# Performance work log

Measured on AMD Instinct MI355X. Metric: run time of the kernel, lower is better.

## Reference

```python
import jax, jax.numpy as jnp
import numpy as np

N, IN, H, C, E = 20000, 256, 256, 16, 640000

def sage_conv(x, edge_index, W_l, b_l, W_r):
    # PyG SAGEConv (aggr='mean', root_weight=True):
    # out = lin_l(mean_{j in N(i)} x_j) + lin_r(x_i)
    src, dst = edge_index[0], edge_index[1]
    n = x.shape[0]
    msgs = x[src]                                            # [E, d] irregular gather
    agg = jax.ops.segment_sum(msgs, dst, num_segments=n)     # [N, d]
    deg = jax.ops.segment_sum(jnp.ones((msgs.shape[0],), x.dtype), dst, num_segments=n)
    agg = agg / jnp.maximum(deg, 1.0)[:, None]               # mean aggregation
    return agg @ W_l + b_l + x @ W_r


def setup_inputs() -> dict:
    key = jax.random.key(0)
    ks = jax.random.split(key, 10)
    s = lambda k, fi, fo: jax.random.normal(k, (fi, fo), jnp.float32) / np.sqrt(fi)
    return {
        "x": jax.random.normal(ks[0], (N, IN), jnp.float32),
        "edge_index": jax.random.randint(ks[1], (2, E), 0, N, jnp.int64),
        "W1l": s(ks[2], IN, H), "b1": jnp.zeros((H,), jnp.float32), "W1r": s(ks[3], IN, H),
        "W2l": s(ks[4], H, H),  "b2": jnp.zeros((H,), jnp.float32), "W2r": s(ks[5], H, H),
        "Wc": s(ks[6], H, C),   "bc": jnp.zeros((C,), jnp.float32),
    }


def reference(x, edge_index, W1l, b1, W1r, W2l, b2, W2r, Wc, bc):
    h = sage_conv(x, edge_index, W1l, b1, W1r)
    h = jax.nn.relu(h)                    # dropout is identity in eval mode
    z = sage_conv(h, edge_index, W2l, b2, W2r)
    return z @ Wc + bc                    # classifier logits [N, C]
```

## Files before the change

### kernel.cpp

```cpp
#include <hip/hip_runtime.h>
#include <hip/hip_bf16.h>


#define FEAT 256
#define NCLS 16
#define ZPAD 264
#define NSH  8
#define SCAP 64
#define SLOTS (NSH * SCAP)
#define CAPTOT 128

typedef __bf16 bf16x8 __attribute__((ext_vector_type(8)));
typedef __bf16 bf16x4 __attribute__((ext_vector_type(4)));
typedef float  f32x4  __attribute__((ext_vector_type(4)));
typedef float  f32x2  __attribute__((ext_vector_type(2)));
typedef unsigned int uint4v __attribute__((ext_vector_type(4)));

#define ACC8(S, U) do {                                                   \
    _Pragma("unroll")                                                     \
    for (int w_ = 0; w_ < 4; ++w_) {                                      \
        f32x2 lo_ = __builtin_amdgcn_cvt_pk_f32_fp8(U[w_], false);        \
        f32x2 hi_ = __builtin_amdgcn_cvt_pk_f32_fp8(U[w_], true);         \
        S[w_][0] += lo_[0]; S[w_][1] += lo_[1];                           \
        S[w_][2] += hi_[0]; S[w_][3] += hi_[1];                           \
    } } while (0)

__device__ __forceinline__ void load_entries(
    const int* __restrict__ cnt, const unsigned short* __restrict__ bucket,
    int node, int lane, int& e0, int& e1, int& deg, float& inv)
{
    int4 ca = *(const int4*)(cnt + node * NSH);
    int4 cb = *(const int4*)(cnt + node * NSH + 4);
    int cs[NSH] = {ca.x, ca.y, ca.z, ca.w, cb.x, cb.y, cb.z, cb.w};
    int ctrue = 0, d = 0;
    #pragma unroll
    for (int s = 0; s < NSH; ++s) {
        ctrue += cs[s];
        cs[s] = cs[s] < SCAP ? cs[s] : SCAP;
        d += cs[s];
    }
    deg = d < CAPTOT ? d : CAPTOT;
    inv = ctrue > 0 ? 1.0f / (float)ctrue : 0.0f;
    const unsigned short* lst = bucket + (size_t)node * SLOTS;

    auto get = [&](int i) -> int {
        int s = 0, loc = i;
        #pragma unroll
        for (int t = 0; t < NSH - 1; ++t) {
            if (s == t && loc >= cs[t]) { loc -= cs[t]; s = t + 1; }
        }
        return lst[s * SCAP + loc];
    };
    e0 = (lane < deg)      ? get(lane)      : 0;
    e1 = (lane + 64 < deg) ? get(lane + 64) : 0;
}


__global__ void combo_kernel(const float* __restrict__ x,
                             const float* __restrict__ W1l, const float* __restrict__ W1r,
                             const float* __restrict__ W2l, const float* __restrict__ W2r,
                             const float* __restrict__ Wc, const float* __restrict__ b2,
                             const float* __restrict__ bc,
                             const int* __restrict__ src, const int* __restrict__ dst,
                             __bf16* __restrict__ xb, unsigned char* __restrict__ x8,
                             __bf16* __restrict__ W1lT, __bf16* __restrict__ W1rT,
                             __bf16* __restrict__ WaT, __bf16* __restrict__ WbT,
                             float* __restrict__ bc2,
                             int* __restrict__ cnt, unsigned short* __restrict__ bucket,
                             int n4, int E, int nb_cvt) {
    int t = threadIdx.x;
    int bx = blockIdx.x;
    if (bx < nb_cvt) {
        int i = bx * 256 + t;
        if (i < n4) {
            f32x4 v = ((const f32x4*)x)[i];
            bf16x4 o;
            #pragma unroll
            for (int j = 0; j < 4; ++j) o[j] = (__bf16)v[j];
            ((bf16x4*)xb)[i] = o;
            int pk = 0;
            pk = __builtin_amdgcn_cvt_pk_fp8_f32(v[0], v[1], pk, false);
            pk = __builtin_amdgcn_cvt_pk_fp8_f32(v[2], v[3], pk, true);
            ((int*)x8)[i] = pk;
        }
    } else if (bx < nb_cvt + 512) {
        int b = bx - nb_cvt;
        int w = b >> 8, nn = b & 255;
        const float* W = w ? W1r : W1l;
        __bf16* WT = w ? W1rT : W1lT;
        WT[nn * FEAT + t] = (__bf16)W[t * FEAT + nn];
    } else if (bx < nb_cvt + 512 + 32) {
        int b = bx - nb_cvt - 512;
        int c = b & 15;
        const float* W = (b < 16) ? W2l : W2r;
        __bf16* WT = (b < 16) ? WaT : WbT;
        float s = 0.f;
        #pragma unroll 4
        for (int m = 0; m < FEAT; ++m)
            s += W[t * FEAT + m] * Wc[m * NCLS + c];
        WT[c * FEAT + t] = (__bf16)s;
    } else if (bx == nb_cvt + 512 + 32) {
        if (t < NCLS) {
            float s = 0.f;
            for (int k = 0; k < FEAT; ++k) s += b2[k] * Wc[k * NCLS + t];
            bc2[t] = s + bc[t];
        }
    } else {
        int sh = bx & (NSH - 1);
        int idx = (bx - nb_cvt - 512 - 33) * 256 + t;
        int e2 = idx * 2;
        if (e2 < E) {
            int2 sv = *(const int2*)(src + e2);
            int2 dv = *(const int2*)(dst + e2);
            int p0 = atomicAdd(&cnt[dv.x * NSH + sh], 1);
            if (p0 < SCAP) bucket[(size_t)dv.x * SLOTS + sh * SCAP + p0] = (unsigned short)sv.x;
            if (e2 + 1 < E) {
                int p1 = atomicAdd(&cnt[dv.y * NSH + sh], 1);
                if (p1 < SCAP) bucket[(size_t)dv.y * SLOTS + sh * SCAP + p1] = (unsigned short)sv.y;
            }
        }
    }
}


__global__ __launch_bounds__(256) void agg_gemm_kernel(
    const unsigned char* __restrict__ t8, const int* __restrict__ cnt,
    const unsigned short* __restrict__ bucket,
    const __bf16* __restrict__ A2,
    const __bf16* __restrict__ B1T, const __bf16* __restrict__ B2T,
    const float* __restrict__ bias,
    const __bf16* __restrict__ WaT, const __bf16* __restrict__ WbT,
    const float* __restrict__ bc2,
    __bf16* __restrict__ pb, float* __restrict__ q, int M)
{
    __shared__ __align__(16) __bf16 tile[32][ZPAD];

    int m0   = blockIdx.x * 32;
    int lane = threadIdx.x & 63;
    int wave = threadIdx.x >> 6;
    int l16  = lane & 15, quad = lane >> 4;

    #pragma unroll 1
    for (int nd = 0; nd < 8; ++nd) {
        int row  = wave * 8 + nd;
        int node = m0 + row;
        if (node < M) {
            int e0, e1, deg; float inv;
            load_entries(cnt, bucket, node, lane, e0, e1, deg, inv);

            f32x4 s0[4], s1[4];
            #pragma unroll
            for (int w = 0; w < 4; ++w) { s0[w] = (f32x4){0.f,0.f,0.f,0.f}; s1[w] = (f32x4){0.f,0.f,0.f,0.f}; }

            int nfull = deg >> 2;
            int rem   = deg & 3;
            const unsigned char* base = t8 + l16 * 16;

            int tt = 0;
            for (; tt + 3 < nfull; tt += 4) {
                int i0 = (tt + 0) * 4 + quad, i1 = (tt + 1) * 4 + quad;
                int i2 = (tt + 2) * 4 + quad, i3 = (tt + 3) * 4 + quad;
                int j0 = (i0 < 64) ? __shfl(e0, i0) : __shfl(e1, i0 - 64);
                int j1 = (i1 < 64) ? __shfl(e0, i1) : __shfl(e1, i1 - 64);
                int j2 = (i2 < 64) ? __shfl(e0, i2) : __shfl(e1, i2 - 64);
                int j3 = (i3 < 64) ? __shfl(e0, i3) : __shfl(e1, i3 - 64);
                uint4v u0 = *(const uint4v*)(base + (size_t)j0 * FEAT);
                uint4v u1 = *(const uint4v*)(base + (size_t)j1 * FEAT);
                uint4v u2 = *(const uint4v*)(base + (size_t)j2 * FEAT);
                uint4v u3 = *(const uint4v*)(base + (size_t)j3 * FEAT);
                ACC8(s0, u0); ACC8(s1, u1); ACC8(s0, u2); ACC8(s1, u3);
            }
            for (; tt < nfull; ++tt) {
                int i = tt * 4 + quad;
                int j = (i < 64) ? __shfl(e0, i) : __shfl(e1, i - 64);
                uint4v u = *(const uint4v*)(base + (size_t)j * FEAT);
                ACC8(s0, u);
            }
            if (rem) {
                int i = nfull * 4 + quad;
                int j = (i < 64) ? __shfl(e0, i) : __shfl(e1, i - 64);
                if (quad < rem) {
                    uint4v u = *(const uint4v*)(base + (size_t)j * FEAT);
                    ACC8(s1, u);
                }
            }

            #pragma unroll
            for (int w = 0; w < 4; ++w)
                #pragma unroll
                for (int j = 0; j < 4; ++j) {
                    float v = s0[w][j] + s1[w][j];
                    v += __shfl_xor(v, 16, 64);
                    v += __shfl_xor(v, 32, 64);
                    s0[w][j] = v;
                }

            bf16x4 o;
            #pragma unroll
            for (int j = 0; j < 4; ++j) o[j] = (__bf16)(s0[quad][j] * inv);
            *(bf16x4*)(&tile[row][l16 * 16 + quad * 4]) = o;
        } else {
            bf16x4 z = (bf16x4){(__bf16)0.f, (__bf16)0.f, (__bf16)0.f, (__bf16)0.f};
            *(bf16x4*)(&tile[row][l16 * 16 + quad * 4]) = z;
        }
    }
    __syncthreads();

    f32x4 acc[2][4];
    #pragma unroll
    for (int a = 0; a < 2; ++a)
        #pragma unroll
        for (int b = 0; b < 4; ++b) acc[a][b] = (f32x4){0.f, 0.f, 0.f, 0.f};

    int arow[2];
    #pragma unroll
    for (int mt = 0; mt < 2; ++mt) {
        int r = m0 + mt * 16 + l16;
        arow[mt] = (r < M) ? r : (M - 1);
    }
    int nbase = wave * 64;

    #pragma unroll 2
    for (int kk = 0; kk < 8; ++kk) {
        int k0 = kk * 32 + quad * 8;
        bf16x8 af[2], bfm[4];
        #pragma unroll
        for (int mt = 0; mt < 2; ++mt)
            af[mt] = *(const bf16x8*)(&tile[mt * 16 + l16][k0]);
        #pragma unroll
        for (int nt = 0; nt < 4; ++nt)
            bfm[nt] = *(const bf16x8*)(B1T + (size_t)(nbase + nt * 16 + l16) * FEAT + k0);
        #pragma unroll
        for (int mt = 0; mt < 2; ++mt)
            #pragma unroll
            for (int nt = 0; nt < 4; ++nt)
                acc[mt][nt] = __builtin_amdgcn_mfma_f32_16x16x32_bf16(
                    af[mt], bfm[nt], acc[mt][nt], 0, 0, 0);
    }
    __syncthreads();

    #pragma unroll 2
    for (int kk = 0; kk < 8; ++kk) {
        int k0 = kk * 32 + quad * 8;
        bf16x8 af[2], bfm[4];
        #pragma unroll
        for (int mt = 0; mt < 2; ++mt)
            af[mt] = *(const bf16x8*)(A2 + (size_t)arow[mt] * FEAT + k0);
        #pragma unroll
        for (int nt = 0; nt < 4; ++nt)
            bfm[nt] = *(const bf16x8*)(B2T + (size_t)(nbase + nt * 16 + l16) * FEAT + k0);
        #pragma unroll
        for (int mt = 0; mt < 2; ++mt)
            #pragma unroll
            for (int nt = 0; nt < 4; ++nt)
                acc[mt][nt] = __builtin_amdgcn_mfma_f32_16x16x32_bf16(
                    af[mt], bfm[nt], acc[mt][nt], 0, 0, 0);
    }

    #pragma unroll
    for (int nt = 0; nt < 4; ++nt) {
        int col = nbase + nt * 16 + l16;
        float bv = bias[col];
        #pragma unroll
        for (int mt = 0; mt < 2; ++mt) {
            int lr = mt * 16 + quad * 4;
            #pragma unroll
            for (int r = 0; r < 4; ++r) {
                float v = acc[mt][nt][r] + bv;
                tile[lr + r][col] = (__bf16)(v > 0.f ? v : 0.f);
            }
        }
    }
    __syncthreads();

    {
        int half = wave >> 1;
        int lr = half * 16 + l16;
        const __bf16* WT = (wave & 1) ? WbT : WaT;
        f32x4 a = {0.f, 0.f, 0.f, 0.f};
        #pragma unroll
        for (int kk = 0; kk < 8; ++kk) {
            int k0 = kk * 32 + quad * 8;
            bf16x8 av = *(const bf16x8*)(&tile[lr][k0]);
            bf16x8 bv = *(const bf16x8*)(WT + (size_t)l16 * FEAT + k0);
            a = __builtin_amdgcn_mfma_f32_16x16x32_bf16(av, bv, a, 0, 0, 0);
        }
        if (wave & 1) {
            float qv = bc2[l16];
            #pragma unroll
            for (int r = 0; r < 4; ++r) {
                int row = m0 + half * 16 + quad * 4 + r;
                if (row < M) q[(size_t)row * NCLS + l16] = a[r] + qv;
            }
        } else {
            #pragma unroll
            for (int r = 0; r < 4; ++r) {
                int row = m0 + half * 16 + quad * 4 + r;
                if (row < M) pb[(size_t)row * NCLS + l16] = (__bf16)a[r];
            }
        }
    }
}


__global__ __launch_bounds__(256) void agg_out_kernel(
    const __bf16* __restrict__ pb, const float* __restrict__ q,
    const int* __restrict__ cnt, const unsigned short* __restrict__ bucket,
    float* __restrict__ out, int n)
{
    int wave = threadIdx.x >> 6;
    int node = blockIdx.x * 4 + wave;
    if (node >= n) return;
    int lane = threadIdx.x & 63;
    int quad = lane >> 4, l16 = lane & 15;

    int e0, e1, deg; float inv;
    load_entries(cnt, bucket, node, lane, e0, e1, deg, inv);

    float s0 = 0.f, s1 = 0.f;
    int nfull = deg >> 2;
    int rem   = deg & 3;

    int tt = 0;
    for (; tt + 3 < nfull; tt += 4) {
        int i0 = (tt + 0) * 4 + quad, i1 = (tt + 1) * 4 + quad;
        int i2 = (tt + 2) * 4 + quad, i3 = (tt + 3) * 4 + quad;
        int j0 = (i0 < 64) ? __shfl(e0, i0) : __shfl(e1, i0 - 64);
        int j1 = (i1 < 64) ? __shfl(e0, i1) : __shfl(e1, i1 - 64);
        int j2 = (i2 < 64) ? __shfl(e0, i2) : __shfl(e1, i2 - 64);
        int j3 = (i3 < 64) ? __shfl(e0, i3) : __shfl(e1, i3 - 64);
        float v0 = (float)pb[(size_t)j0 * NCLS + l16];
        float v1 = (float)pb[(size_t)j1 * NCLS + l16];
        float v2 = (float)pb[(size_t)j2 * NCLS + l16];
        float v3 = (float)pb[(size_t)j3 * NCLS + l16];
        s0 += v0 + v1;
        s1 += v2 + v3;
    }
    for (; tt < nfull; ++tt) {
        int i = tt * 4 + quad;
        int j = (i < 64) ? __shfl(e0, i) : __shfl(e1, i - 64);
        s0 += (float)pb[(size_t)j * NCLS + l16];
    }
    if (rem) {
        int i = nfull * 4 + quad;
        int j = (i < 64) ? __shfl(e0, i) : __shfl(e1, i - 64);
        if (quad < rem) s1 += (float)pb[(size_t)j * NCLS + l16];
    }

    float v = s0 + s1;
    v += __shfl_xor(v, 16, 64);
    v += __shfl_xor(v, 32, 64);

    if (quad == 0) {
        out[(size_t)node * NCLS + l16] = v * inv + q[(size_t)node * NCLS + l16];
    }
}


extern "C" void kernel_launch(void* const* d_in, const int* in_sizes, int n_in,
                              void* d_out, int out_size, void* d_ws, size_t ws_size,
                              hipStream_t stream) {
    const float* x   = (const float*)d_in[0];
    const int*   ei  = (const int*)d_in[1];
    const float* W1l = (const float*)d_in[2];
    const float* b1  = (const float*)d_in[3];
    const float* W1r = (const float*)d_in[4];
    const float* W2l = (const float*)d_in[5];
    const float* b2  = (const float*)d_in[6];
    const float* W2r = (const float*)d_in[7];
    const float* Wc  = (const float*)d_in[8];
    const float* bc  = (const float*)d_in[9];
    float* out = (float*)d_out;

    const int n = in_sizes[0] / FEAT;
    const int E = in_sizes[1] / 2;
    const int* srcp = ei;
    const int* dstp = ei + E;

    char* p = (char*)d_ws;
    auto alloc = [&](size_t bytes) { char* r = p; p += (bytes + 511) & ~511ull; return r; };
    int* cnt       = (int*)alloc((size_t)n * NSH * 4);
    unsigned short* bucket = (unsigned short*)alloc((size_t)n * SLOTS * 2);
    __bf16* W1lT   = (__bf16*)alloc((size_t)FEAT * FEAT * 2);
    __bf16* W1rT   = (__bf16*)alloc((size_t)FEAT * FEAT * 2);
    __bf16* WaT    = (__bf16*)alloc((size_t)NCLS * FEAT * 2);
    __bf16* WbT    = (__bf16*)alloc((size_t)NCLS * FEAT * 2);
    float*  bc2    = (float*)alloc((size_t)NCLS * 4);
    __bf16* xb     = (__bf16*)alloc((size_t)n * FEAT * 2);
    unsigned char* x8 = (unsigned char*)alloc((size_t)n * FEAT);
    __bf16* pb     = (__bf16*)alloc((size_t)n * NCLS * 2);
    float*  qb     = (float*)alloc((size_t)n * NCLS * 4);

    int n4 = n * FEAT / 4;
    int nb_cvt  = (n4 + 255) / 256;
    int nb_edge = (E + 511) / 512;

    hipMemsetAsync(cnt, 0, (size_t)n * NSH * 4, stream);

    combo_kernel<<<nb_cvt + 512 + 32 + 1 + nb_edge, 256, 0, stream>>>(
        x, W1l, W1r, W2l, W2r, Wc, b2, bc, srcp, dstp,
        xb, x8, W1lT, W1rT, WaT, WbT, bc2, cnt, bucket, n4, E, nb_cvt);

    agg_gemm_kernel<<<(n + 31) / 32, 256, 0, stream>>>(
        x8, cnt, bucket, xb, W1lT, W1rT, b1, WaT, WbT, bc2, pb, qb, n);

    agg_out_kernel<<<(n + 3) / 4, 256, 0, stream>>>(pb, qb, cnt, bucket, out, n);
}
```

Before: 221.2 us.

## Halve agg_gemm row tile and overlap root GEMM with aggregation barrier

Shrinks the per-block row tile of the fused aggregate+GEMM kernel from 32 to 16 nodes, doubling the grid to improve load balance and occupancy across CUs. It also moves the root-weight GEMM (x @ W_r from global memory) ahead of the first barrier so it runs before waiting for the shared-memory aggregation tile. The trade-off is that weight matrices get reloaded by twice as many blocks, and only two of four waves do the final classifier projection.

After: 208.5 us. 1.06x faster.

```diff
diff --git a/kernel.cpp b/kernel.cpp
--- a/kernel.cpp
+++ b/kernel.cpp
@@ -5,6 +5,7 @@
 #define FEAT 256
 #define NCLS 16
 #define ZPAD 264
+#define MT   16
 #define NSH  8
 #define SCAP 64
 #define SLOTS (NSH * SCAP)
@@ -133,16 +134,16 @@
     const float* __restrict__ bc2,
     __bf16* __restrict__ pb, float* __restrict__ q, int M)
 {
-    __shared__ __align__(16) __bf16 tile[32][ZPAD];
-
-    int m0   = blockIdx.x * 32;
+    __shared__ __align__(16) __bf16 tile[MT][ZPAD];
+
+    int m0   = blockIdx.x * MT;
     int lane = threadIdx.x & 63;
     int wave = threadIdx.x >> 6;
     int l16  = lane & 15, quad = lane >> 4;
 
     #pragma unroll 1
-    for (int nd = 0; nd < 8; ++nd) {
-        int row  = wave * 8 + nd;
+    for (int nd = 0; nd < 4; ++nd) {
+        int row  = wave * 4 + nd;
         int node = m0 + row;
         if (node < M) {
             int e0, e1, deg; float inv;
@@ -204,99 +205,79 @@
             *(bf16x4*)(&tile[row][l16 * 16 + quad * 4]) = z;
         }
     }
-    __syncthreads();
-
-    f32x4 acc[2][4];
+
+    f32x4 acc[4];
     #pragma unroll
-    for (int a = 0; a < 2; ++a)
-        #pragma unroll
-        for (int b = 0; b < 4; ++b) acc[a][b] = (f32x4){0.f, 0.f, 0.f, 0.f};
-
-    int arow[2];
-    #pragma unroll
-    for (int mt = 0; mt < 2; ++mt) {
-        int r = m0 + mt * 16 + l16;
-        arow[mt] = (r < M) ? r : (M - 1);
-    }
+    for (int b = 0; b < 4; ++b) acc[b] = (f32x4){0.f, 0.f, 0.f, 0.f};
+
+    int r = m0 + l16;
+    int arow = (r < M) ? r : (M - 1);
     int nbase = wave * 64;
 
     #pragma unroll 2
     for (int kk = 0; kk < 8; ++kk) {
         int k0 = kk * 32 + quad * 8;
-        bf16x8 af[2], bfm[4];
-        #pragma unroll
-        for (int mt = 0; mt < 2; ++mt)
-            af[mt] = *(const bf16x8*)(&tile[mt * 16 + l16][k0]);
+        bf16x8 af = *(const bf16x8*)(A2 + (size_t)arow * FEAT + k0);
+        bf16x8 bfm[4];
         #pragma unroll
         for (int nt = 0; nt < 4; ++nt)
-            bfm[nt] = *(const bf16x8*)(B1T + (size_t)(nbase + nt * 16 + l16) * FEAT + k0);
-        #pragma unroll
-        for (int mt = 0; mt < 2; ++mt)
-            #pragma unroll
-            for (int nt = 0; nt < 4; ++nt)
-                acc[mt][nt] = __builtin_amdgcn_mfma_f32_16x16x32_bf16(
-                    af[mt], bfm[nt], acc[mt][nt], 0, 0, 0);
-    }
+            bfm[nt] = *(const bf16x8*)(B2T + (size_t)(nbase + nt * 16 + l16) * FEAT + k0);
+        #pragma unroll
+        for (int nt = 0; nt < 4; ++nt)
+            acc[nt] = __builtin_amdgcn_mfma_f32_16x16x32_bf16(af, bfm[nt], acc[nt], 0, 0, 0);
+    }
+
     __syncthreads();
 
     #pragma unroll 2
     for (int kk = 0; kk < 8; ++kk) {
         int k0 = kk * 32 + quad * 8;
-        bf16x8 af[2], bfm[4];
-        #pragma unroll
-        for (int mt = 0; mt < 2; ++mt)
-            af[mt] = *(const bf16x8*)(A2 + (size_t)arow[mt] * FEAT + k0);
+        bf16x8 af = *(const bf16x8*)(&tile[l16][k0]);
+        bf16x8 bfm[4];
         #pragma unroll
         for (int nt = 0; nt < 4; ++nt)
-            bfm[nt] = *(const bf16x8*)(B2T + (size_t)(nbase + nt * 16 + l16) * FEAT + k0);
-        #pragma unroll
-        for (int mt = 0; mt < 2; ++mt)
-            #pragma unroll
-            for (int nt = 0; nt < 4; ++nt)
-                acc[mt][nt] = __builtin_amdgcn_mfma_f32_16x16x32_bf16(
-                    af[mt], bfm[nt], acc[mt][nt], 0, 0, 0);
-    }
+            bfm[nt] = *(const bf16x8*)(B1T + (size_t)(nbase + nt * 16 + l16) * FEAT + k0);
+        #pragma unroll
+        for (int nt = 0; nt < 4; ++nt)
+            acc[nt] = __builtin_amdgcn_mfma_f32_16x16x32_bf16(af, bfm[nt], acc[nt], 0, 0, 0);
+    }
+    __syncthreads();
 
     #pragma unroll
     for (int nt = 0; nt < 4; ++nt) {
         int col = nbase + nt * 16 + l16;
         float bv = bias[col];
-        #pragma unroll
-        for (int mt = 0; mt < 2; ++mt) {
-            int lr = mt * 16 + quad * 4;
-            #pragma unroll
-            for (int r = 0; r < 4; ++r) {
-                float v = acc[mt][nt][r] + bv;
-                tile[lr + r][col] = (__bf16)(v > 0.f ? v : 0.f);
-            }
+        int lr = quad * 4;
+        #pragma unroll
+        for (int rr = 0; rr < 4; ++rr) {
+            float v = acc[nt][rr] + bv;
+            tile[lr + rr][col] = (__bf16)(v > 0.f ? v : 0.f);
         }
     }
     __syncthreads();
 
-    {
-        int half = wave >> 1;
-        int lr = half * 16 + l16;
-        const __bf16* WT = (wave & 1) ? WbT : WaT;
+    if (wave < 2) {
+        const __bf16* WT = wave ? WbT : WaT;
         f32x4 a = {0.f, 0.f, 0.f, 0.f};
         #pragma unroll
         for (int kk = 0; kk < 8; ++kk) {
             int k0 = kk * 32 + quad * 8;
-            bf16x8 av = *(const bf16x8*)(&tile[lr][k0]);
+            bf16x8 av = *(const bf16x8*)(&tile[l16][k0]);
             bf16x8 bv = *(const bf16x8*)(WT + (size_t)l16 * FEAT + k0);
             a = __builtin_amdgcn_mfma_f32_16x16x32_bf16(av, bv, a, 0, 0, 0);
         }
-        if (wave & 1) {
+        if (wave) {
             float qv = bc2[l16];
             #pragma unroll
-            for (int r = 0; r < 4; ++r) {
-                int row = m0 + half * 16 + quad * 4 + r;
-                if (row < M) q[(size_t)row * NCLS + l16] = a[r] + qv;
+            for (int rr = 0; rr < 4; ++rr) {
+                int row = m0 + quad * 4 + rr;
+                if (row < M) q[(size_t)row * NCLS + l16] = a[rr] + qv;
             }
         } else {
             #pragma unroll
-            for (int r = 0; r < 4; ++r) {
-                int row = m0 + half * 16 + quad * 4 + r;
-                if (row < M) pb[(size_t)row * NCLS + l16] = (__bf16)a[r];
+            for (int rr = 0; rr < 4; ++rr) {
+                int row = m0 + quad * 4 + rr;
+                if (row < M) pb[(size_t)row * NCLS + l16] = (__bf16)a[rr];
             }
         }
     }
@@ -401,7 +382,7 @@
         x, W1l, W1r, W2l, W2r, Wc, b2, bc, srcp, dstp,
         xb, x8, W1lT, W1rT, WaT, WbT, bc2, cnt, bucket, n4, E, nb_cvt);
 
-    agg_gemm_kernel<<<(n + 31) / 32, 256, 0, stream>>>(
+    agg_gemm_kernel<<<(n + MT - 1) / MT, 256, 0, stream>>>(
         x8, cnt, bucket, xb, W1lT, W1rT, b1, WaT, WbT, bc2, pb, qb, n);
 
     agg_out_kernel<<<(n + 3) / 4, 256, 0, stream>>>(pb, qb, cnt, bucket, out, n);
```
